# Kernel tuning notes

Measured on AMD Instinct MI355X. Metric: run time of the kernel, lower is better.

## Reference

```python
import jax, jax.numpy as jnp
import numpy as np

B, T, C, H = 8, 1024, 768, 12
HD = C // H  # 64

def setup_inputs() -> dict:
    key = jax.random.key(0)
    ks = jax.random.split(key, 5)
    s = 0.02
    return {
        "x": jax.random.normal(ks[0], (B, T, C), dtype=jnp.float32),
        "w_attn": jax.random.normal(ks[1], (C, 3 * C), dtype=jnp.float32) * s,
        "b_attn": jnp.zeros((3 * C,), dtype=jnp.float32),
        "w_proj": jax.random.normal(ks[2], (C, C), dtype=jnp.float32) * s,
        "b_proj": jnp.zeros((C,), dtype=jnp.float32),
    }

def reference(x, w_attn, b_attn, w_proj, b_proj):
    Bx, Tx, Cx = x.shape
    qkv = x @ w_attn + b_attn                      # [B,T,3C]
    q, k, v = jnp.split(qkv, 3, axis=-1)
    # [B,H,T,hd]
    q = q.reshape(Bx, Tx, H, HD).transpose(0, 2, 1, 3)
    k = k.reshape(Bx, Tx, H, HD).transpose(0, 2, 1, 3)
    v = v.reshape(Bx, Tx, H, HD).transpose(0, 2, 1, 3)
    scale = 1.0 / jnp.sqrt(jnp.asarray(HD, dtype=x.dtype))
    scores = jnp.einsum('bhqd,bhkd->bhqk', q, k) * scale  # [B,H,T,T]
    causal = jnp.tril(jnp.ones((Tx, Tx), dtype=bool))
    scores = jnp.where(causal, scores, jnp.asarray(-jnp.inf, dtype=x.dtype))
    weights = jax.nn.softmax(scores, axis=-1)
    y = jnp.einsum('bhqk,bhkd->bhqd', weights, v)  # [B,H,T,hd]
    y = y.transpose(0, 2, 1, 3).reshape(Bx, Tx, Cx)
    return y @ w_proj + b_proj
```

## Files before the change

### kernel.cpp

```cpp
#include <hip/hip_runtime.h>
#include <cstdint>
#include <cstddef>

#define B_  8
#define T_  1024
#define C_  768
#define H_  12
#define HD_ 64
#define K3_ 2304

typedef unsigned short u16;
typedef __attribute__((ext_vector_type(8))) short bf16x8;
typedef __attribute__((ext_vector_type(4))) float f32x4;

#define MFMA __builtin_amdgcn_mfma_f32_16x16x32_bf16

__device__ __forceinline__ u16 f2bf(float f) {
    unsigned u = __builtin_bit_cast(unsigned, f);
    u += 0x7fffu + ((u >> 16) & 1u);
    return (u16)(u >> 16);
}

__device__ __forceinline__ unsigned pk2bf(float a, float b) {
    unsigned ua = __builtin_bit_cast(unsigned, a) + 0x8000u;
    unsigned ub = __builtin_bit_cast(unsigned, b) + 0x8000u;
    return (ua >> 16) | (ub & 0xffff0000u);
}

#define GLL16(gp, lp) __builtin_amdgcn_global_load_lds( \
    (__attribute__((address_space(1))) unsigned int*)(gp), \
    (__attribute__((address_space(3))) unsigned int*)(lp), 16, 0, 0)

__device__ __forceinline__ void tcvt_tile(const float* __restrict__ in, u16* __restrict__ out,
                                          int R, int Cc, int bx, int by, int tid, float* tile ) {
    int bc = bx * 32, br = by * 32;
    int tx = tid & 31, ty = tid >> 5;
    #pragma unroll
    for (int kk = 0; kk < 32; kk += 8)
        tile[(ty + kk) * 33 + tx] = in[(size_t)(br + ty + kk) * Cc + bc + tx];
    __syncthreads();
    #pragma unroll
    for (int kk = 0; kk < 32; kk += 8)
        out[(size_t)(bc + ty + kk) * R + br + tx] = f2bf(tile[tx * 33 + ty + kk]);
}

__global__ void prep(const float* __restrict__ x, u16* __restrict__ xb,
                     const float* __restrict__ wa, u16* __restrict__ wat,
                     const float* __restrict__ wp, u16* __restrict__ wpt) {
    __shared__ float tile[32 * 33];
    int bid = blockIdx.x, tid = threadIdx.x;
    if (bid < 6144) {
        int i = bid * 256 + tid;
        float4 v = ((const float4*)x)[i];
        ushort4 o;
        o.x = f2bf(v.x); o.y = f2bf(v.y); o.z = f2bf(v.z); o.w = f2bf(v.w);
        ((ushort4*)xb)[i] = o;
    } else if (bid < 6144 + 1728) {
        int b = bid - 6144;
        tcvt_tile(wa, wat, C_, K3_, b % 72, b / 72, tid, tile);
    } else {
        int b = bid - 7872;
        tcvt_tile(wp, wpt, C_, C_, b % 24, b / 24, tid, tile);
    }
}

#define VMW6 asm volatile("s_waitcnt vmcnt(6)" ::: "memory")
#define VMW0 asm volatile("s_waitcnt vmcnt(0)" ::: "memory")
#define BAR  __builtin_amdgcn_s_barrier()

__device__ __forceinline__ void gemm_pipe(const u16* __restrict__ A, const u16* __restrict__ Bt,
                                          int m0, int n0, u16* SM, f32x4 (&acc)[4][4]) {
    const int K = C_;
    int tid = threadIdx.x;
    int lane = tid & 63, wv = tid >> 6;
    int wr = wv >> 2, wc = wv & 3;
    int r16 = lane & 15, quad = lane >> 4;
    int sw = r16 & 7;
    int x0 = (quad ^ sw) * 8;
    int x1 = ((4 + quad) ^ sw) * 8;
    int arow = (wr * 64 + r16) * 64;
    int brow = (wc * 64 + r16) * 64;
    int tr = tid >> 3;
    int tb = (tid & 7) ^ (tr & 7);
    const u16* Ag = A  + (size_t)(m0 + tr) * K + tb * 8;
    const u16* Bg = Bt + (size_t)(n0 + tr) * K + tb * 8;
    u16* SLa = SM + tid * 8;
    u16* SLb = SM + 24576 + tid * 8;
    const u16* SMB = SM + 24576;

#define STG_A(ss, kO, u)  GLL16(Ag + (size_t)(u) * 64 * K + (kO), SLa + (ss) * 8192 + (u) * 4096)
#define STG_B(ss, kO, u)  GLL16(Bg + (size_t)(u) * 64 * K + (kO), SLb + (ss) * 16384 + (u) * 4096)
#define STG_H0(ss, kO) { STG_A(ss, kO, 0); STG_A(ss, kO, 1); STG_B(ss, kO, 0); }
#define STG_H1(ss, kO) { STG_B(ss, kO, 1); STG_B(ss, kO, 2); STG_B(ss, kO, 3); }
#define RD(rs, XC) { \
    const u16* Ar_ = SM  + (rs) * 8192  + arow; \
    const u16* Br_ = SMB + (rs) * 16384 + brow; \
    _Pragma("unroll") for (int i_ = 0; i_ < 4; i_++) af[i_] = *(const bf16x8*)&Ar_[i_ * 1024 + (XC)]; \
    _Pragma("unroll") for (int j_ = 0; j_ < 4; j_++) bb[j_] = *(const bf16x8*)&Br_[j_ * 1024 + (XC)]; }
#define MM() { \
    __builtin_amdgcn_s_setprio(1); \
    _Pragma("unroll") for (int i_ = 0; i_ < 4; i_++) \
    _Pragma("unroll") for (int j_ = 0; j_ < 4; j_++) \
        acc[i_][j_] = MFMA(af[i_], bb[j_], acc[i_][j_], 0, 0, 0); \
    __builtin_amdgcn_s_setprio(0); }

    STG_H0(0, 0);  STG_H1(0, 0);
    STG_H0(1, 64); STG_H1(1, 64);
    VMW6; BAR;

    int sa = 0, sb = 1, sc = 2;
    int kS = 128;
    for (int it = 0; it < 5; ++it) {
        bf16x8 af[4], bb[4];
        RD(sa, x0); STG_H0(sc, kS);            BAR; MM(); BAR;
        RD(sa, x1); STG_H1(sc, kS);      VMW6; BAR; MM(); BAR;
        RD(sb, x0); STG_H0(sa, kS + 64);       BAR; MM(); BAR;
        RD(sb, x1); STG_H1(sa, kS + 64); VMW6; BAR; MM(); BAR;
        int t_ = sa; sa = sc; sc = sb; sb = t_;
        kS += 128;
    }
    {
        bf16x8 af[4], bb[4];
        RD(sa, x0); MM();
        RD(sa, x1); MM();
        VMW0; BAR;
        RD(sb, x0); MM();
        RD(sb, x1); MM();
    }
#undef STG_A
#undef STG_B
#undef STG_H0
#undef STG_H1
#undef RD
#undef MM
}

__launch_bounds__(512)
__global__ void gemm_qkv(const u16* __restrict__ A, const u16* __restrict__ Bt,
                         const float* __restrict__ bias,
                         u16* __restrict__ q, u16* __restrict__ k, u16* __restrict__ v) {
    __shared__ __align__(16) u16 SM[73728];
    int id = blockIdx.x;
    int xcd = id & 7, j = id >> 3;
    int m0 = (xcd * 8 + (j & 7)) * 128;
    int n0 = (j >> 3) * 256;
    f32x4 acc[4][4] = {};
    gemm_pipe(A, Bt, m0, n0, SM, acc);

    int tid = threadIdx.x;
    int lane = tid & 63, wv = tid >> 6;
    int wr = wv >> 2, wc = wv & 3;
    int r16 = lane & 15, quad = lane >> 4;
    __syncthreads();

    int sec = n0 / C_;
    int cc0 = n0 - sec * C_;
    int b = m0 >> 10, t0 = m0 & 1023;

    if (sec == 2) {
        #pragma unroll
        for (int i = 0; i < 4; i++) {
            #pragma unroll
            for (int jj = 0; jj < 4; jj++) {
                int cc = cc0 + wc * 64 + jj * 16 + r16;
                float bv = bias[2 * C_ + cc];
                int h = cc >> 6, hd = cc & 63;
                int t = t0 + wr * 64 + i * 16 + quad * 4;
                ushort4 ov;
                ov.x = f2bf(acc[i][jj][0] + bv); ov.y = f2bf(acc[i][jj][1] + bv);
                ov.z = f2bf(acc[i][jj][2] + bv); ov.w = f2bf(acc[i][jj][3] + bv);
                *(ushort4*)(v + (((size_t)b * H_ + h) * HD_ + hd) * T_ + t) = ov;
            }
        }
    } else {
        float scale = (sec == 0) ? 0.125f : 1.0f;
        u16* dst = (sec == 0) ? q : k;
        u16 (*Cs)[136] = (u16(*)[136])SM;
        #pragma unroll
        for (int half = 0; half < 2; half++) {
            if ((wc >> 1) == half) {
                #pragma unroll
                for (int i = 0; i < 4; i++)
                    #pragma unroll
                    for (int jj = 0; jj < 4; jj++) {
                        int col = (wc & 1) * 64 + jj * 16 + r16;
                        float bv = bias[sec * C_ + cc0 + half * 128 + col];
                        #pragma unroll
                        for (int r = 0; r < 4; r++)
                            Cs[wr * 64 + i * 16 + quad * 4 + r][col] = f2bf((acc[i][jj][r] + bv) * scale);
                    }
            }
            __syncthreads();
            int rsel = tid >> 4;
            int ch = tid & 15;
            int hh = (cc0 + half * 128 + ch * 8) >> 6;
            int hd0 = (ch & 7) * 8;
            #pragma unroll
            for (int p = 0; p < 4; p++) {
                int rl = p * 32 + rsel;
                uint4 val = *(const uint4*)&Cs[rl][ch * 8];
                *(uint4*)(dst + (((size_t)b * H_ + hh) * T_ + t0 + rl) * HD_ + hd0) = val;
            }
            __syncthreads();
        }
    }
}

__launch_bounds__(512)
__global__ void gemm_proj(const u16* __restrict__ A, const u16* __restrict__ Bt,
                          const float* __restrict__ bias, float* __restrict__ out) {
    __shared__ __align__(16) u16 SM[73728];
    int id = blockIdx.x;
    int xcd = id & 7, j = id >> 3;
    int m0 = (xcd * 8 + (j & 7)) * 128;
    int n0 = (j >> 3) * 256;
    f32x4 acc[4][4] = {};
    gemm_pipe(A, Bt, m0, n0, SM, acc);

    int tid = threadIdx.x;
    int lane = tid & 63, wv = tid >> 6;
    int wr = wv >> 2, wc = wv & 3;
    int r16 = lane & 15, quad = lane >> 4;
    #pragma unroll
    for (int i = 0; i < 4; i++) {
        #pragma unroll
        for (int jj = 0; jj < 4; jj++) {
            int gn = n0 + wc * 64 + jj * 16 + r16;
            float bv = bias[gn];
            #pragma unroll
            for (int r = 0; r < 4; r++) {
                int gm = m0 + wr * 64 + i * 16 + quad * 4 + r;
                out[(size_t)gm * C_ + gn] = acc[i][jj][r] + bv;
            }
        }
    }
}

__launch_bounds__(256, 2)
__global__ void attn(const u16* __restrict__ q, const u16* __restrict__ k,
                     const u16* __restrict__ v, u16* __restrict__ y) {
    __shared__ __align__(16) u16 Kb[2][64][64];
    __shared__ __align__(16) u16 Vb[2][64][64];
    __shared__ __align__(16) u16 P[4][2][16][72];
    int tid = threadIdx.x, lane = tid & 63, w = tid >> 6;
    int r16 = lane & 15, quad = lane >> 4;
    int id = blockIdx.x;
    int bh = id % 96;
    int bi = id / 96;
    int b = bh / H_, h = bh - b * H_;
    int x = bi * 4 + w;
    int t_lo = x, t_hi = 63 - x;
    int qb_lo = t_lo * 16, qb_hi = t_hi * 16;
    const u16* qh = q + (size_t)bh * T_ * HD_;
    const u16* kh = k + (size_t)bh * T_ * HD_;
    const u16* vh = v + (size_t)bh * HD_ * T_;

    bf16x8 ql0 = *(const bf16x8*)(qh + (size_t)(qb_lo + r16) * HD_ + quad * 8);
    bf16x8 ql1 = *(const bf16x8*)(qh + (size_t)(qb_lo + r16) * HD_ + 32 + quad * 8);
    bf16x8 qh0 = *(const bf16x8*)(qh + (size_t)(qb_hi + r16) * HD_ + quad * 8);
    bf16x8 qh1 = *(const bf16x8*)(qh + (size_t)(qb_hi + r16) * HD_ + 32 + quad * 8);

    f32x4 oL[4] = {}, oH[4] = {};
    float lL = 0.f, lH = 0.f;
    int qyL = qb_lo + r16, qyH = qb_hi + r16;
    int ilo_last = bi;
    int n64 = __builtin_amdgcn_readfirstlane(16 - bi);

    int srow = lane >> 3;
    int scb  = (lane & 7) ^ srow;
    const u16* kst = kh + (size_t)(w * 16 + srow) * HD_ + scb * 8;
    const u16* vst = vh + (size_t)(w * 16 + srow) * T_ + scb * 8;
    int swz = (r16 & 7);

    {
        #pragma unroll
        for (int s2 = 0; s2 < 2; s2++) {
            GLL16(kst + (size_t)(s2 * 8) * HD_, &Kb[0][w * 16 + s2 * 8][0] + lane * 8);
            GLL16(vst + (size_t)(s2 * 8) * T_,  &Vb[0][w * 16 + s2 * 8][0] + lane * 8);
        }
    }
    __syncthreads();

    for (int it = 0; it < n64; ++it) {
        int kv0 = it * 64;
        int buf = it & 1;
        bool lo_on = (it <= ilo_last);
        if (it + 1 < n64) {
            int kvn = kv0 + 64;
            #pragma unroll
            for (int s2 = 0; s2 < 2; s2++) {
                GLL16(kst + (size_t)(kvn + s2 * 8) * HD_, &Kb[buf ^ 1][w * 16 + s2 * 8][0] + lane * 8);
                GLL16(vst + (size_t)(s2 * 8) * T_ + kvn,  &Vb[buf ^ 1][w * 16 + s2 * 8][0] + lane * 8);
            }
        }
        bf16x8 kf[4][2];
        #pragma unroll
        for (int n = 0; n < 4; n++)
            #pragma unroll
            for (int c = 0; c < 2; c++)
                kf[n][c] = *(const bf16x8*)&Kb[buf][n * 16 + r16][((c * 4 + quad) ^ swz) * 8];
        f32x4 sH[4] = {};
        #pragma unroll
        for (int n = 0; n < 4; n++) {
            sH[n] = MFMA(kf[n][0], qh0, sH[n], 0, 0, 0);
            sH[n] = MFMA(kf[n][1], qh1, sH[n], 0, 0, 0);
        }
        if (it == n64 - 1) {
            #pragma unroll
            for (int n = 0; n < 4; n++)
                #pragma unroll
                for (int r = 0; r < 4; r++)
                    if (kv0 + n * 16 + quad * 4 + r > qyH) sH[n][r] = -1e30f;
        }
        #pragma unroll
        for (int n = 0; n < 4; n++) {
            float p0 = __expf(sH[n][0]);
            float p1 = __expf(sH[n][1]);
            float p2 = __expf(sH[n][2]);
            float p3 = __expf(sH[n][3]);
            lH += (p0 + p1) + (p2 + p3);
            uint2 pd; pd.x = pk2bf(p0, p1); pd.y = pk2bf(p2, p3);
            *(uint2*)&P[w][1][r16][n * 16 + quad * 4] = pd;
        }
        if (lo_on) {
            f32x4 sL[4] = {};
            #pragma unroll
            for (int n = 0; n < 4; n++) {
                sL[n] = MFMA(kf[n][0], ql0, sL[n], 0, 0, 0);
                sL[n] = MFMA(kf[n][1], ql1, sL[n], 0, 0, 0);
            }
            if (it == ilo_last) {
                #pragma unroll
                for (int n = 0; n < 4; n++)
                    #pragma unroll
                    for (int r = 0; r < 4; r++)
                        if (kv0 + n * 16 + quad * 4 + r > qyL) sL[n][r] = -1e30f;
            }
            #pragma unroll
            for (int n = 0; n < 4; n++) {
                float p0 = __expf(sL[n][0]);
                float p1 = __expf(sL[n][1]);
                float p2 = __expf(sL[n][2]);
                float p3 = __expf(sL[n][3]);
                lL += (p0 + p1) + (p2 + p3);
                uint2 pd; pd.x = pk2bf(p0, p1); pd.y = pk2bf(p2, p3);
                *(uint2*)&P[w][0][r16][n * 16 + quad * 4] = pd;
            }
        }
        bf16x8 vf[4][2];
        #pragma unroll
        for (int j = 0; j < 4; j++)
            #pragma unroll
            for (int c = 0; c < 2; c++)
                vf[j][c] = *(const bf16x8*)&Vb[buf][j * 16 + r16][((c * 4 + quad) ^ swz) * 8];
        #pragma unroll
        for (int c = 0; c < 2; c++) {
            bf16x8 pfH = *(const bf16x8*)&P[w][1][r16][c * 32 + quad * 8];
            #pragma unroll
            for (int j = 0; j < 4; j++)
                oH[j] = MFMA(vf[j][c], pfH, oH[j], 0, 0, 0);
        }
        if (lo_on) {
            #pragma unroll
            for (int c = 0; c < 2; c++) {
                bf16x8 pfL = *(const bf16x8*)&P[w][0][r16][c * 32 + quad * 8];
                #pragma unroll
                for (int j = 0; j < 4; j++)
                    oL[j] = MFMA(vf[j][c], pfL, oL[j], 0, 0, 0);
            }
        }
        __syncthreads();
    }

    lH += __shfl_xor(lH, 16, 64);
    lH += __shfl_xor(lH, 32, 64);
    lL += __shfl_xor(lL, 16, 64);
    lL += __shfl_xor(lL, 32, 64);
    float invH = 1.f / lH, invL = 1.f / lL;
    int tqH = qb_hi + r16, tqL = qb_lo + r16;
    #pragma unroll
    for (int j = 0; j < 4; j++) {
        ushort4 ovH, ovL;
        ovH.x = f2bf(oH[j][0] * invH); ovH.y = f2bf(oH[j][1] * invH);
        ovH.z = f2bf(oH[j][2] * invH); ovH.w = f2bf(oH[j][3] * invH);
        ovL.x = f2bf(oL[j][0] * invL); ovL.y = f2bf(oL[j][1] * invL);
        ovL.z = f2bf(oL[j][2] * invL); ovL.w = f2bf(oL[j][3] * invL);
        *(ushort4*)(y + ((size_t)b * T_ + tqH) * C_ + h * 64 + j * 16 + quad * 4) = ovH;
        *(ushort4*)(y + ((size_t)b * T_ + tqL) * C_ + h * 64 + j * 16 + quad * 4) = ovL;
    }
}

extern "C" void kernel_launch(void* const* d_in, const int* in_sizes, int n_in,
                              void* d_out, int out_size, void* d_ws, size_t ws_size,
                              hipStream_t stream) {
    const float* x      = (const float*)d_in[0];
    const float* w_attn = (const float*)d_in[1];
    const float* b_attn = (const float*)d_in[2];
    const float* w_proj = (const float*)d_in[3];
    const float* b_proj = (const float*)d_in[4];
    float* out = (float*)d_out;

    char* ws = (char*)d_ws;
    size_t off = 0;
    auto alloc = [&](size_t bytes) {
        void* p = ws + off;
        off += (bytes + 255) & ~(size_t)255;
        return p;
    };
    const size_t M = (size_t)B_ * T_;
    u16* x_bf = (u16*)alloc(M * C_ * 2);
    u16* wat  = (u16*)alloc((size_t)K3_ * C_ * 2);
    u16* wpt  = (u16*)alloc((size_t)C_ * C_ * 2);
    u16* qb   = (u16*)alloc((size_t)B_ * H_ * T_ * HD_ * 2);
    u16* kb   = (u16*)alloc((size_t)B_ * H_ * T_ * HD_ * 2);
    u16* vb   = (u16*)alloc((size_t)B_ * H_ * T_ * HD_ * 2);
    u16* yb   = (u16*)alloc(M * C_ * 2);

    prep<<<6144 + 1728 + 576, 256, 0, stream>>>(x, x_bf, w_attn, wat, w_proj, wpt);
    gemm_qkv<<<576, 512, 0, stream>>>(x_bf, wat, b_attn, qb, kb, vb);
    attn<<<8 * 96, 256, 0, stream>>>(qb, kb, vb, yb);
    gemm_proj<<<192, 512, 0, stream>>>(yb, wpt, b_proj, out);
}
```

Before: 168.7 us.

## Shrink GEMM N-tile to 192 and restructure K pipeline into full-tile phases

Both GEMMs now use 128x192 tiles instead of 128x256, with each wave covering 48 columns. This raises the grid from 576 to 768 blocks for QKV and from 192 to 256 for proj, which fills the 256 CUs more evenly. The K loop is rewritten so each phase stages a whole 64-wide K slice with 5 loads and one wait and barrier, instead of two half-phases with extra barriers. The QKV epilogue writes three heads per tile in a single LDS pass. The cost is less B reuse per tile and a different pipeline depth.

Measured after the change: 159.2 us (median of 2 runs). 1.06x faster.

```diff
diff --git a/kernel.cpp b/kernel.cpp
--- a/kernel.cpp
+++ b/kernel.cpp
@@ -64,12 +64,12 @@
     }
 }
 
-#define VMW6 asm volatile("s_waitcnt vmcnt(6)" ::: "memory")
+#define VMW5 asm volatile("s_waitcnt vmcnt(5)" ::: "memory")
 #define VMW0 asm volatile("s_waitcnt vmcnt(0)" ::: "memory")
 #define BAR  __builtin_amdgcn_s_barrier()
 
 __device__ __forceinline__ void gemm_pipe(const u16* __restrict__ A, const u16* __restrict__ Bt,
-                                          int m0, int n0, u16* SM, f32x4 (&acc)[4][4]) {
+                                          int m0, int n0, u16* SM, f32x4 (&acc)[4][3]) {
     const int K = C_;
     int tid = threadIdx.x;
     int lane = tid & 63, wv = tid >> 6;
@@ -79,7 +79,7 @@
     int x0 = (quad ^ sw) * 8;
     int x1 = ((4 + quad) ^ sw) * 8;
     int arow = (wr * 64 + r16) * 64;
-    int brow = (wc * 64 + r16) * 64;
+    int brow = (wc * 48 + r16) * 64;
     int tr = tid >> 3;
     int tb = (tid & 7) ^ (tr & 7);
     const u16* Ag = A  + (size_t)(m0 + tr) * K + tb * 8;
@@ -88,64 +88,70 @@
     u16* SLb = SM + 24576 + tid * 8;
     const u16* SMB = SM + 24576;
 
-#define STG_A(ss, kO, u)  GLL16(Ag + (size_t)(u) * 64 * K + (kO), SLa + (ss) * 8192 + (u) * 4096)
-#define STG_B(ss, kO, u)  GLL16(Bg + (size_t)(u) * 64 * K + (kO), SLb + (ss) * 16384 + (u) * 4096)
-#define STG_H0(ss, kO) { STG_A(ss, kO, 0); STG_A(ss, kO, 1); STG_B(ss, kO, 0); }
-#define STG_H1(ss, kO) { STG_B(ss, kO, 1); STG_B(ss, kO, 2); STG_B(ss, kO, 3); }
-#define RD(rs, XC) { \
+#define STG_T(ss, kO) { \
+    GLL16(Ag + (kO),                       SLa + (ss) * 8192); \
+    GLL16(Ag + (size_t)64 * K + (kO),      SLa + (ss) * 8192 + 4096); \
+    GLL16(Bg + (kO),                       SLb + (ss) * 12288); \
+    GLL16(Bg + (size_t)64 * K + (kO),      SLb + (ss) * 12288 + 4096); \
+    GLL16(Bg + (size_t)128 * K + (kO),     SLb + (ss) * 12288 + 8192); }
+#define RDH(rs, XC, af, bf) { \
     const u16* Ar_ = SM  + (rs) * 8192  + arow; \
-    const u16* Br_ = SMB + (rs) * 16384 + brow; \
+    const u16* Br_ = SMB + (rs) * 12288 + brow; \
     _Pragma("unroll") for (int i_ = 0; i_ < 4; i_++) af[i_] = *(const bf16x8*)&Ar_[i_ * 1024 + (XC)]; \
-    _Pragma("unroll") for (int j_ = 0; j_ < 4; j_++) bb[j_] = *(const bf16x8*)&Br_[j_ * 1024 + (XC)]; }
-#define MM() { \
+    _Pragma("unroll") for (int j_ = 0; j_ < 3; j_++) bf[j_] = *(const bf16x8*)&Br_[j_ * 1024 + (XC)]; }
+#define MMH(af, bf) { \
     __builtin_amdgcn_s_setprio(1); \
     _Pragma("unroll") for (int i_ = 0; i_ < 4; i_++) \
-    _Pragma("unroll") for (int j_ = 0; j_ < 4; j_++) \
-        acc[i_][j_] = MFMA(af[i_], bb[j_], acc[i_][j_], 0, 0, 0); \
+    _Pragma("unroll") for (int j_ = 0; j_ < 3; j_++) \
+        acc[i_][j_] = MFMA(af[i_], bf[j_], acc[i_][j_], 0, 0, 0); \
     __builtin_amdgcn_s_setprio(0); }
-
-    STG_H0(0, 0);  STG_H1(0, 0);
-    STG_H0(1, 64); STG_H1(1, 64);
-    VMW6; BAR;
-
-    int sa = 0, sb = 1, sc = 2;
+#define PHASE(rs, ts, kO) { \
+    bf16x8 a0[4], b0[3], a1[4], b1[3]; \
+    RDH(rs, x0, a0, b0); RDH(rs, x1, a1, b1); \
+    STG_T(ts, kO); \
+    MMH(a0, b0); MMH(a1, b1); \
+    VMW5; BAR; }
+
+    STG_T(0, 0); STG_T(1, 64);
+    VMW5; BAR;
+
     int kS = 128;
-    for (int it = 0; it < 5; ++it) {
-        bf16x8 af[4], bb[4];
-        RD(sa, x0); STG_H0(sc, kS);            BAR; MM(); BAR;
-        RD(sa, x1); STG_H1(sc, kS);      VMW6; BAR; MM(); BAR;
-        RD(sb, x0); STG_H0(sa, kS + 64);       BAR; MM(); BAR;
-        RD(sb, x1); STG_H1(sa, kS + 64); VMW6; BAR; MM(); BAR;
-        int t_ = sa; sa = sc; sc = sb; sb = t_;
-        kS += 128;
-    }
+    #pragma unroll
+    for (int o = 0; o < 3; ++o) {
+        PHASE(0, 2, kS);
+        PHASE(1, 0, kS + 64);
+        PHASE(2, 1, kS + 128);
+        kS += 192;
+    }
+    PHASE(0, 2, 704);
     {
-        bf16x8 af[4], bb[4];
-        RD(sa, x0); MM();
-        RD(sa, x1); MM();
+        bf16x8 a0[4], b0[3], a1[4], b1[3];
+        RDH(1, x0, a0, b0); RDH(1, x1, a1, b1);
+        MMH(a0, b0); MMH(a1, b1);
         VMW0; BAR;
-        RD(sb, x0); MM();
-        RD(sb, x1); MM();
-    }
-#undef STG_A
-#undef STG_B
-#undef STG_H0
-#undef STG_H1
-#undef RD
-#undef MM
+    }
+    {
+        bf16x8 a0[4], b0[3], a1[4], b1[3];
+        RDH(2, x0, a0, b0); RDH(2, x1, a1, b1);
+        MMH(a0, b0); MMH(a1, b1);
+    }
+#undef STG_T
+#undef RDH
+#undef MMH
+#undef PHASE
 }
 
 __launch_bounds__(512)
 __global__ void gemm_qkv(const u16* __restrict__ A, const u16* __restrict__ Bt,
                          const float* __restrict__ bias,
                          u16* __restrict__ q, u16* __restrict__ k, u16* __restrict__ v) {
-    __shared__ __align__(16) u16 SM[73728];
+    __shared__ __align__(16) u16 SM[61440];
     int id = blockIdx.x;
     int xcd = id & 7, j = id >> 3;
     int m0 = (xcd * 8 + (j & 7)) * 128;
-    int n0 = (j >> 3) * 256;
-    f32x4 acc[4][4] = {};
-    gemm_pipe(A, Bt, m0, n0, SM, acc);
+    int np = j >> 3;
+    f32x4 acc[4][3] = {};
+    gemm_pipe(A, Bt, m0, np * 192, SM, acc);
 
     int tid = threadIdx.x;
     int lane = tid & 63, wv = tid >> 6;
@@ -153,16 +159,16 @@
     int r16 = lane & 15, quad = lane >> 4;
     __syncthreads();
 
-    int sec = n0 / C_;
-    int cc0 = n0 - sec * C_;
+    int sec = np >> 2;
+    int cc0 = (np & 3) * 192;
     int b = m0 >> 10, t0 = m0 & 1023;
 
     if (sec == 2) {
         #pragma unroll
         for (int i = 0; i < 4; i++) {
             #pragma unroll
-            for (int jj = 0; jj < 4; jj++) {
-                int cc = cc0 + wc * 64 + jj * 16 + r16;
+            for (int jj = 0; jj < 3; jj++) {
+                int cc = cc0 + wc * 48 + jj * 16 + r16;
                 float bv = bias[2 * C_ + cc];
                 int h = cc >> 6, hd = cc & 63;
                 int t = t0 + wr * 64 + i * 16 + quad * 4;
@@ -175,46 +181,41 @@
     } else {
         float scale = (sec == 0) ? 0.125f : 1.0f;
         u16* dst = (sec == 0) ? q : k;
-        u16 (*Cs)[136] = (u16(*)[136])SM;
-        #pragma unroll
-        for (int half = 0; half < 2; half++) {
-            if ((wc >> 1) == half) {
+        u16 (*Cs)[200] = (u16(*)[200])SM;
+        #pragma unroll
+        for (int i = 0; i < 4; i++)
+            #pragma unroll
+            for (int jj = 0; jj < 3; jj++) {
+                int col = wc * 48 + jj * 16 + r16;
+                float bv = bias[sec * C_ + cc0 + col];
                 #pragma unroll
-                for (int i = 0; i < 4; i++)
-                    #pragma unroll
-                    for (int jj = 0; jj < 4; jj++) {
-                        int col = (wc & 1) * 64 + jj * 16 + r16;
-                        float bv = bias[sec * C_ + cc0 + half * 128 + col];
-                        #pragma unroll
-                        for (int r = 0; r < 4; r++)
-                            Cs[wr * 64 + i * 16 + quad * 4 + r][col] = f2bf((acc[i][jj][r] + bv) * scale);
-                    }
-            }
-            __syncthreads();
-            int rsel = tid >> 4;
-            int ch = tid & 15;
-            int hh = (cc0 + half * 128 + ch * 8) >> 6;
-            int hd0 = (ch & 7) * 8;
-            #pragma unroll
-            for (int p = 0; p < 4; p++) {
-                int rl = p * 32 + rsel;
-                uint4 val = *(const uint4*)&Cs[rl][ch * 8];
-                *(uint4*)(dst + (((size_t)b * H_ + hh) * T_ + t0 + rl) * HD_ + hd0) = val;
-            }
-            __syncthreads();
-        }
+                for (int r = 0; r < 4; r++)
+                    Cs[wr * 64 + i * 16 + quad * 4 + r][col] = f2bf((acc[i][jj][r] + bv) * scale);
+            }
+        __syncthreads();
+        int h0 = cc0 >> 6;
+        int rsel = tid >> 3;
+        int ch = tid & 7;
+        #pragma unroll
+        for (int p = 0; p < 2; p++)
+            #pragma unroll
+            for (int h3 = 0; h3 < 3; h3++) {
+                int rl = p * 64 + rsel;
+                uint4 val = *(const uint4*)&Cs[rl][h3 * 64 + ch * 8];
+                *(uint4*)(dst + (((size_t)b * H_ + h0 + h3) * T_ + t0 + rl) * HD_ + ch * 8) = val;
+            }
     }
 }
 
 __launch_bounds__(512)
 __global__ void gemm_proj(const u16* __restrict__ A, const u16* __restrict__ Bt,
                           const float* __restrict__ bias, float* __restrict__ out) {
-    __shared__ __align__(16) u16 SM[73728];
+    __shared__ __align__(16) u16 SM[61440];
     int id = blockIdx.x;
     int xcd = id & 7, j = id >> 3;
     int m0 = (xcd * 8 + (j & 7)) * 128;
-    int n0 = (j >> 3) * 256;
-    f32x4 acc[4][4] = {};
+    int n0 = (j >> 3) * 192;
+    f32x4 acc[4][3] = {};
     gemm_pipe(A, Bt, m0, n0, SM, acc);
 
     int tid = threadIdx.x;
@@ -224,8 +225,8 @@
     #pragma unroll
     for (int i = 0; i < 4; i++) {
         #pragma unroll
-        for (int jj = 0; jj < 4; jj++) {
-            int gn = n0 + wc * 64 + jj * 16 + r16;
+        for (int jj = 0; jj < 3; jj++) {
+            int gn = n0 + wc * 48 + jj * 16 + r16;
             float bv = bias[gn];
             #pragma unroll
             for (int r = 0; r < 4; r++) {
@@ -417,7 +418,7 @@
     u16* yb   = (u16*)alloc(M * C_ * 2);
 
     prep<<<6144 + 1728 + 576, 256, 0, stream>>>(x, x_bf, w_attn, wat, w_proj, wpt);
-    gemm_qkv<<<576, 512, 0, stream>>>(x_bf, wat, b_attn, qb, kb, vb);
+    gemm_qkv<<<768, 512, 0, stream>>>(x_bf, wat, b_attn, qb, kb, vb);
     attn<<<8 * 96, 256, 0, stream>>>(qb, kb, vb, yb);
-    gemm_proj<<<192, 512, 0, stream>>>(yb, wpt, b_proj, out);
-}
+    gemm_proj<<<256, 512, 0, stream>>>(yb, wpt, b_proj, out);
+}
```
